# Optimization experiments

Measured on AMD Instinct MI355X. Metric: run time of the kernel, lower is better.

Reference implementation:

```python
import jax, jax.numpy as jnp
import numpy as np

B, T, C, H = 2, 2048, 1024, 16
HD = C // H            # 64
LAYER_IDX, N_LAYER = 5, 12
BASE = 16
# window_mode='power_2.0': progress=(5+1)/12=0.5; window=max(16, int(16+0.5**2*(2048-16)))=524
WINDOW = max(BASE, int(BASE + ((LAYER_IDX + 1) / N_LAYER) ** 2.0 * (T - BASE)))
WINDOW = min(WINDOW, T)


def setup_inputs() -> dict:
    key = jax.random.key(0)
    ks = jax.random.split(key, 6)
    x = jax.random.normal(ks[0], (B, T, C), dtype=jnp.float32)
    Wq = jax.random.normal(ks[1], (C, C), dtype=jnp.float32) * 0.02
    Wk = jax.random.normal(ks[2], (C, C), dtype=jnp.float32) * 0.02
    Wv = jax.random.normal(ks[3], (C, C), dtype=jnp.float32) * 0.02
    Wo = jax.random.normal(ks[4], (C, C), dtype=jnp.float32) * 0.02
    # RoPE tables: angles theta_i = t / 10000^(i/(HD/2)), shape (T,1,HD//2) to broadcast over (B,T,H,HD//2)
    half = HD // 2
    inv_freq = 1.0 / (10000.0 ** (jnp.arange(half, dtype=jnp.float32) / half))
    ang = jnp.arange(T, dtype=jnp.float32)[:, None] * inv_freq[None, :]  # (T, half)
    rope_cos = jnp.cos(ang)[:, None, :]  # (T,1,half)
    rope_sin = jnp.sin(ang)[:, None, :]
    return {"x": x, "Wq": Wq, "Wk": Wk, "Wv": Wv, "Wo": Wo,
            "rope_cos": rope_cos, "rope_sin": rope_sin}


def _apply_rotary(x, cos, sin):
    d = x.shape[-1] // 2
    x1, x2 = x[..., :d], x[..., d:]
    return jnp.concatenate([x1 * cos + x2 * sin, -x2 * sin + x1 * cos], axis=-1)


def reference(x, Wq, Wk, Wv, Wo, rope_cos, rope_sin):
    Bv, Tv, Cv = x.shape
    q = (x @ Wq).reshape(Bv, Tv, H, HD)
    k = (x @ Wk).reshape(Bv, Tv, H, HD)
    v = (x @ Wv).reshape(Bv, Tv, H, HD)
    q = _apply_rotary(q, rope_cos, rope_sin)
    k = _apply_rotary(k, rope_cos, rope_sin)
    # sliding-window causal mask: cols<=rows and cols>=rows-WINDOW+1
    rows = jnp.arange(Tv)[:, None]
    cols = jnp.arange(Tv)[None, :]
    allowed = (cols <= rows) & (cols >= rows - WINDOW + 1)  # (T,T)
    scale = 1.0 / np.sqrt(HD)
    scores = jnp.einsum('bthd,bshd->bhts', q, k) * scale  # (B,H,T,T)
    scores = jnp.where(allowed[None, None], scores, -jnp.inf)
    attn = jax.nn.softmax(scores, axis=-1)
    y = jnp.einsum('bhts,bshd->bthd', attn, v).reshape(Bv, Tv, Cv)
    return y @ Wo
```

## Files before the change

kernel.cpp:

```cpp
#include <hip/hip_runtime.h>
#include <math.h>

typedef unsigned short u16;
typedef unsigned int u32;
typedef __bf16 bf16x8 __attribute__((ext_vector_type(8)));
typedef float f32x4 __attribute__((ext_vector_type(4)));
typedef unsigned short ushort4v __attribute__((ext_vector_type(4)));

#define T_SEQ 2048
#define WIN_M1 523
#define QSCALE 0.180336879f
#define MASKV -1e30f

__device__ __forceinline__ u16 f2b(float f) {
  union { float f; unsigned int u; } v; v.f = f;
  unsigned int u = v.u;
  u += 0x7FFFu + ((u >> 16) & 1u);
  return (u16)(u >> 16);
}

__device__ __forceinline__ u32 cvtpk(float lo, float hi) {
  u32 r;
  asm("v_cvt_pk_bf16_f32 %0, %1, %2" : "=v"(r) : "v"(lo), "v"(hi));
  return r;
}

__device__ __forceinline__ void load_lds16(const u16* g, u16* l) {
  __builtin_amdgcn_global_load_lds(
      (const __attribute__((address_space(1))) void*)g,
      (__attribute__((address_space(3))) void*)l, 16, 0, 0);
}

__global__ void prep_k(const float* __restrict__ x, u16* __restrict__ xb,
                       const float* __restrict__ W0, const float* __restrict__ W1,
                       const float* __restrict__ W2, const float* __restrict__ W3,
                       u16* __restrict__ WcatT, u16* __restrict__ WoT) {
  const int bid = blockIdx.x;
  if (bid < 4096) {
    int i = bid * 256 + threadIdx.x;
    float4 v = ((const float4*)x)[i];
    u16* d = xb + i * 4;
    d[0] = f2b(v.x); d[1] = f2b(v.y); d[2] = f2b(v.z); d[3] = f2b(v.w);
    return;
  }
  __shared__ float tile[32][33];
  const int t = bid - 4096;
  const int z = t >> 10, i = t & 1023;
  const float* W = (z == 0) ? W0 : (z == 1) ? W1 : (z == 2) ? W2 : W3;
  u16* Wt = (z < 3) ? (WcatT + (size_t)z * 1024 * 1024) : WoT;
  int tx = threadIdx.x & 31, ty = threadIdx.x >> 5;
  int n0 = (i & 31) * 32, k0 = (i >> 5) * 32;
#pragma unroll
  for (int j = 0; j < 4; ++j)
    tile[ty + j * 8][tx] = W[(size_t)(k0 + ty + j * 8) * 1024 + n0 + tx];
  __syncthreads();
#pragma unroll
  for (int j = 0; j < 4; ++j)
    Wt[(size_t)(n0 + ty + j * 8) * 1024 + k0 + tx] = f2b(tile[tx][ty + j * 8]);
}

template <int MODE>
__global__ __launch_bounds__(256, 4) void gemm_k(
    const u16* __restrict__ A, const u16* __restrict__ Bt,
    float* __restrict__ outf,
    u16* __restrict__ Qo, u16* __restrict__ Ko, u16* __restrict__ Vto,
    const float* __restrict__ rc, const float* __restrict__ rs) {
  __shared__ alignas(16) u16 As[2][128 * 32];
  __shared__ alignas(16) u16 Bs[2][128 * 32];
  const int tid = threadIdx.x, lane = tid & 63, w = tid >> 6;
  const int l15 = lane & 15, q4 = lane >> 4;
  const int row0 = blockIdx.y * 128, col0 = blockIdx.x * 128;
  const int wm = w >> 1, wn = w & 1;
  constexpr int NT = 32;

  f32x4 acc[4][4];
#pragma unroll
  for (int i = 0; i < 4; ++i)
#pragma unroll
    for (int j = 0; j < 4; ++j) acc[i][j] = (f32x4){0.f, 0.f, 0.f, 0.f};

  const int off0 = (w * 2) * 1024 + lane * 16;
  const int r0 = off0 >> 6, c0 = (off0 & 63) >> 1;
  const int off1 = off0 + 1024;
  const int r1 = off1 >> 6, c1 = (off1 & 63) >> 1;
  const u16* gA0 = A + (size_t)(row0 + r0) * 1024 + c0;
  const u16* gA1 = A + (size_t)(row0 + r1) * 1024 + c1;
  const u16* gB0 = Bt + (size_t)(col0 + r0) * 1024 + c0;
  const u16* gB1 = Bt + (size_t)(col0 + r1) * 1024 + c1;
  const int soff = (w * 2) * 512;

  auto stage = [&](int buf, int t) {
    const int k0 = t * 32;
    load_lds16(gA0 + k0, &As[buf][soff]);
    load_lds16(gA1 + k0, &As[buf][soff + 512]);
    load_lds16(gB0 + k0, &Bs[buf][soff]);
    load_lds16(gB1 + k0, &Bs[buf][soff + 512]);
  };
  auto compute = [&](int buf) {
    bf16x8 af[4], bfr[4];
#pragma unroll
    for (int im = 0; im < 4; ++im)
      af[im] = *(const bf16x8*)&As[buf][(wm * 64 + im * 16 + l15) * 32 + q4 * 8];
#pragma unroll
    for (int jn = 0; jn < 4; ++jn)
      bfr[jn] = *(const bf16x8*)&Bs[buf][(wn * 64 + jn * 16 + l15) * 32 + q4 * 8];
#pragma unroll
    for (int im = 0; im < 4; ++im)
#pragma unroll
      for (int jn = 0; jn < 4; ++jn)
        acc[im][jn] = __builtin_amdgcn_mfma_f32_16x16x32_bf16(af[im], bfr[jn], acc[im][jn], 0, 0, 0);
  };

  stage(0, 0);
  for (int t = 0; t + 1 < NT; ++t) {
    stage((t + 1) & 1, t + 1);
    asm volatile("s_waitcnt vmcnt(4)" ::: "memory");
    __builtin_amdgcn_s_barrier();
    compute(t & 1);
    __builtin_amdgcn_s_barrier();
  }
  asm volatile("s_waitcnt vmcnt(0)" ::: "memory");
  __builtin_amdgcn_s_barrier();
  compute((NT - 1) & 1);

  if constexpr (MODE == 0) {
#pragma unroll
    for (int im = 0; im < 4; ++im) {
      const int rowb = row0 + wm * 64 + im * 16 + q4 * 4;
      const int b = rowb >> 11, t0 = rowb & 2047;
#pragma unroll
      for (int jn = 0; jn < 2; ++jn) {
        const int n = col0 + wn * 64 + jn * 16 + l15;
        const int sel = n >> 10, nn = n & 1023;
        const int h = nn >> 6, hd = nn & 63;
        if (sel < 2) {
          const float qs = (sel == 0) ? QSCALE : 1.0f;
          u16* dst = (sel == 0 ? Qo : Ko) + ((size_t)(b * 16 + h) * 2048) * 64;
#pragma unroll
          for (int r = 0; r < 4; ++r) {
            const int tt = t0 + r;
            const float c = rc[tt * 32 + hd], s = rs[tt * 32 + hd];
            const float x1 = acc[im][jn][r], x2 = acc[im][jn + 2][r];
            dst[(size_t)tt * 64 + hd] = f2b((x1 * c + x2 * s) * qs);
            dst[(size_t)tt * 64 + hd + 32] = f2b((x1 * c - x2 * s) * qs);
          }
        } else {
          ushort4v p1, p2;
#pragma unroll
          for (int r = 0; r < 4; ++r) {
            p1[r] = f2b(acc[im][jn][r]);
            p2[r] = f2b(acc[im][jn + 2][r]);
          }
          u16* dst = Vto + (size_t)(b * 16 + h) * 64 * 2048 + t0;
          *(ushort4v*)(dst + (size_t)hd * 2048) = p1;
          *(ushort4v*)(dst + (size_t)(hd + 32) * 2048) = p2;
        }
      }
    }
  } else {
#pragma unroll
    for (int im = 0; im < 4; ++im) {
      const int rowb = row0 + wm * 64 + im * 16 + q4 * 4;
#pragma unroll
      for (int jn = 0; jn < 4; ++jn) {
        const int n = col0 + wn * 64 + jn * 16 + l15;
#pragma unroll
        for (int r = 0; r < 4; ++r)
          outf[(size_t)(rowb + r) * 1024 + n] = acc[im][jn][r];
      }
    }
  }
}

__global__ __launch_bounds__(256) void attn_k(
    const u16* __restrict__ Q, const u16* __restrict__ Kk,
    const u16* __restrict__ Vt, u16* __restrict__ Y) {
  const int lane = threadIdx.x & 63, w = threadIdx.x >> 6;
  const int l15 = lane & 15, q4 = lane >> 4;
  const int hw = blockIdx.x;
  const int work = (hw & 7) * 64 + (hw >> 3);
  const int bh = work >> 4;
  const int qt = 15 - (work & 15);
  const int q0 = qt * 128 + w * 32;
  const u16* Qb = Q + (size_t)bh * 2048 * 64;
  const u16* Kb = Kk + (size_t)bh * 2048 * 64;
  const u16* Vb = Vt + (size_t)bh * 64 * 2048;

  bf16x8 bq[2][2];
#pragma unroll
  for (int qs = 0; qs < 2; ++qs)
#pragma unroll
    for (int kb = 0; kb < 2; ++kb)
      bq[qs][kb] = *(const bf16x8*)(Qb + (size_t)(q0 + qs * 16 + l15) * 64 + kb * 32 + q4 * 8);

  f32x4 o[2][4];
#pragma unroll
  for (int qs = 0; qs < 2; ++qs)
#pragma unroll
    for (int jo = 0; jo < 4; ++jo) o[qs][jo] = (f32x4){0.f, 0.f, 0.f, 0.f};
  float lp[2] = {0.f, 0.f};

  int s0 = q0 - WIN_M1; if (s0 < 0) s0 = 0; s0 &= ~31;
  const int srcA = l15 + ((q4 & 1) << 5);
  const int srcB = srcA + 16;
  const bool lowq4 = (q4 < 2);

  bf16x8 kc[2][2], kn[2][2];
  bf16x8 vc[4], vn[4];
#pragma unroll
  for (int ks = 0; ks < 2; ++ks)
#pragma unroll
    for (int kb = 0; kb < 2; ++kb)
      kc[ks][kb] = *(const bf16x8*)(Kb + (size_t)(s0 + ks * 16 + l15) * 64 + kb * 32 + q4 * 8);
#pragma unroll
  for (int jo = 0; jo < 4; ++jo)
    vc[jo] = *(const bf16x8*)(Vb + (size_t)(jo * 16 + l15) * 2048 + s0 + q4 * 8);

  int kv0 = s0;

#define TILE_BODY(KC, VC, KN, VN)                                                      \
  {                                                                                    \
    const int kvn = kv0 + 32;                                                          \
    if (kvn <= q0) {                                                                   \
      _Pragma("unroll") for (int ks = 0; ks < 2; ++ks)                                 \
          _Pragma("unroll") for (int kb = 0; kb < 2; ++kb)                             \
              KN[ks][kb] = *(const bf16x8*)(Kb + (size_t)(kvn + ks * 16 + l15) * 64 +  \
                                            kb * 32 + q4 * 8);                         \
      _Pragma("unroll") for (int jo = 0; jo < 4; ++jo)                                 \
          VN[jo] = *(const bf16x8*)(Vb + (size_t)(jo * 16 + l15) * 2048 + kvn +        \
                                    q4 * 8);                                           \
    }                                                                                  \
    f32x4 ss[2][2];                                                                    \
    _Pragma("unroll") for (int ks = 0; ks < 2; ++ks)                                   \
        _Pragma("unroll") for (int qs = 0; qs < 2; ++qs)                               \
            ss[ks][qs] = (f32x4){0.f, 0.f, 0.f, 0.f};                                  \
    _Pragma("unroll") for (int kb = 0; kb < 2; ++kb)                                   \
        _Pragma("unroll") for (int ks = 0; ks < 2; ++ks)                               \
            _Pragma("unroll") for (int qs = 0; qs < 2; ++qs)                           \
                ss[ks][qs] = __builtin_amdgcn_mfma_f32_16x16x32_bf16(                  \
                    KC[ks][kb], bq[qs][kb], ss[ks][qs], 0, 0, 0);                      \
    if ((kv0 + 32 > q0) || (kv0 < q0 - 492)) {                                         \
      _Pragma("unroll") for (int qs = 0; qs < 2; ++qs) {                               \
        const int tq = q0 + qs * 16 + l15;                                             \
        _Pragma("unroll") for (int ks = 0; ks < 2; ++ks)                               \
            _Pragma("unroll") for (int r = 0; r < 4; ++r) {                            \
          const int kv = kv0 + ks * 16 + q4 * 4 + r;                                   \
          if (kv > tq || kv < tq - WIN_M1) ss[ks][qs][r] = MASKV;                      \
        }                                                                              \
      }                                                                                \
    }                                                                                  \
    _Pragma("unroll") for (int qs = 0; qs < 2; ++qs) {                                 \
      float p[2][4];                                                                   \
      _Pragma("unroll") for (int ks = 0; ks < 2; ++ks)                                 \
          _Pragma("unroll") for (int r = 0; r < 4; ++r)                                \
              p[ks][r] = exp2f(ss[ks][qs][r]);                                         \
      lp[qs] += ((p[0][0] + p[0][1]) + (p[0][2] + p[0][3])) +                          \
                ((p[1][0] + p[1][1]) + (p[1][2] + p[1][3]));                           \
      const u32 a0 = cvtpk(p[0][0], p[0][1]), a1 = cvtpk(p[0][2], p[0][3]);            \
      const u32 b0 = cvtpk(p[1][0], p[1][1]), b1 = cvtpk(p[1][2], p[1][3]);            \
      union { u32 d[4]; bf16x8 v; } pu;                                                \
      const u32 d0a = (u32)__shfl((int)a0, srcA), d0b = (u32)__shfl((int)b0, srcA);    \
      const u32 d1a = (u32)__shfl((int)a1, srcA), d1b = (u32)__shfl((int)b1, srcA);    \
      const u32 d2a = (u32)__shfl((int)a0, srcB), d2b = (u32)__shfl((int)b0, srcB);    \
      const u32 d3a = (u32)__shfl((int)a1, srcB), d3b = (u32)__shfl((int)b1, srcB);    \
      pu.d[0] = lowq4 ? d0a : d0b;                                                     \
      pu.d[1] = lowq4 ? d1a : d1b;                                                     \
      pu.d[2] = lowq4 ? d2a : d2b;                                                     \
      pu.d[3] = lowq4 ? d3a : d3b;                                                     \
      _Pragma("unroll") for (int jo = 0; jo < 4; ++jo)                                 \
          o[qs][jo] = __builtin_amdgcn_mfma_f32_16x16x32_bf16(pu.v, VC[jo],            \
                                                              o[qs][jo], 0, 0, 0);     \
    }                                                                                  \
  }

  while (true) {
    TILE_BODY(kc, vc, kn, vn);
    kv0 += 32; if (kv0 > q0) break;
    TILE_BODY(kn, vn, kc, vc);
    kv0 += 32; if (kv0 > q0) break;
  }
#undef TILE_BODY

  const int b = bh >> 4, h = bh & 15;
  u16* Yb = Y + (size_t)(b * 2048 + q0) * 1024 + h * 64 + l15;
#pragma unroll
  for (int qs = 0; qs < 2; ++qs) {
    float l = lp[qs];
    l += __shfl_xor(l, 16);
    l += __shfl_xor(l, 32);
#pragma unroll
    for (int r = 0; r < 4; ++r) {
      const float lv = __shfl(l, q4 * 4 + r);
      const float inv = 1.0f / lv;
      u16* yr = Yb + (size_t)(qs * 16 + q4 * 4 + r) * 1024;
#pragma unroll
      for (int jo = 0; jo < 4; ++jo) yr[jo * 16] = f2b(o[qs][jo][r] * inv);
    }
  }
}

extern "C" void kernel_launch(void* const* d_in, const int* in_sizes, int n_in,
                              void* d_out, int out_size, void* d_ws, size_t ws_size,
                              hipStream_t stream) {
  const float* x = (const float*)d_in[0];
  const float* Wq = (const float*)d_in[1];
  const float* Wk = (const float*)d_in[2];
  const float* Wv = (const float*)d_in[3];
  const float* Wo = (const float*)d_in[4];
  const float* rc = (const float*)d_in[5];
  const float* rs = (const float*)d_in[6];
  float* out = (float*)d_out;
  char* ws = (char*)d_ws;
  const size_t MB = 1024 * 1024;
  u16* xb = (u16*)(ws);
  u16* WcatT = (u16*)(ws + 8 * MB);
  u16* WoT = (u16*)(ws + 14 * MB);
  u16* Qr = (u16*)(ws + 16 * MB);
  u16* Kr = (u16*)(ws + 24 * MB);
  u16* Vt = (u16*)(ws + 32 * MB);
  u16* Y = (u16*)(ws + 40 * MB);

  prep_k<<<8192, 256, 0, stream>>>(x, xb, Wq, Wk, Wv, Wo, WcatT, WoT);
  gemm_k<0><<<dim3(24, 32), 256, 0, stream>>>(xb, WcatT, nullptr, Qr, Kr, Vt, rc, rs);
  attn_k<<<512, 256, 0, stream>>>(Qr, Kr, Vt, Y);
  gemm_k<1><<<dim3(8, 32), 256, 0, stream>>>(Y, WoT, out, nullptr, nullptr, nullptr, nullptr, nullptr);
}
```

Baseline: 108.3 us.

## Split attention KV range across two blocks and triple-buffer GEMM LDS

Attention work is split into two halves of the key range per query tile, doubling the grid; each half writes unnormalized bf16 partial outputs and row sums, and a new combine kernel adds them and normalizes. This targets low occupancy and load imbalance in the attention kernel. The GEMM mainloop moves from double to triple LDS buffering with deeper prefetch to hide global load latency. The cost is an extra kernel launch, extra memory traffic, bf16 rounding of partial sums, and more LDS per GEMM block.

```diff
diff --git a/kernel.cpp b/kernel.cpp
--- a/kernel.cpp
+++ b/kernel.cpp
@@ -6,6 +6,7 @@
 typedef __bf16 bf16x8 __attribute__((ext_vector_type(8)));
 typedef float f32x4 __attribute__((ext_vector_type(4)));
 typedef unsigned short ushort4v __attribute__((ext_vector_type(4)));
+typedef unsigned short ushort8v __attribute__((ext_vector_type(8)));
 
 #define T_SEQ 2048
 #define WIN_M1 523
@@ -17,6 +18,12 @@
   unsigned int u = v.u;
   u += 0x7FFFu + ((u >> 16) & 1u);
   return (u16)(u >> 16);
+}
+
+__device__ __forceinline__ float b2f(u16 b) {
+  union { unsigned int u; float f; } v;
+  v.u = ((u32)b) << 16;
+  return v.f;
 }
 
 __device__ __forceinline__ u32 cvtpk(float lo, float hi) {
@@ -65,8 +72,8 @@
     float* __restrict__ outf,
     u16* __restrict__ Qo, u16* __restrict__ Ko, u16* __restrict__ Vto,
     const float* __restrict__ rc, const float* __restrict__ rs) {
-  __shared__ alignas(16) u16 As[2][128 * 32];
-  __shared__ alignas(16) u16 Bs[2][128 * 32];
+  __shared__ alignas(16) u16 As[3][128 * 32];
+  __shared__ alignas(16) u16 Bs[3][128 * 32];
   const int tid = threadIdx.x, lane = tid & 63, w = tid >> 6;
   const int l15 = lane & 15, q4 = lane >> 4;
   const int row0 = blockIdx.y * 128, col0 = blockIdx.x * 128;
@@ -112,16 +119,25 @@
   };
 
   stage(0, 0);
-  for (int t = 0; t + 1 < NT; ++t) {
-    stage((t + 1) & 1, t + 1);
-    asm volatile("s_waitcnt vmcnt(4)" ::: "memory");
+  stage(1, 1);
+  int bs = 2, bc = 0;
+  for (int t = 0; t + 2 < NT; ++t) {
+    stage(bs, t + 2);
+    asm volatile("s_waitcnt vmcnt(8)" ::: "memory");
     __builtin_amdgcn_s_barrier();
-    compute(t & 1);
+    compute(bc);
     __builtin_amdgcn_s_barrier();
-  }
+    bs = (bs + 1 == 3) ? 0 : bs + 1;
+    bc = (bc + 1 == 3) ? 0 : bc + 1;
+  }
+  asm volatile("s_waitcnt vmcnt(4)" ::: "memory");
+  __builtin_amdgcn_s_barrier();
+  compute(bc);
+  __builtin_amdgcn_s_barrier();
+  bc = (bc + 1 == 3) ? 0 : bc + 1;
   asm volatile("s_waitcnt vmcnt(0)" ::: "memory");
   __builtin_amdgcn_s_barrier();
-  compute((NT - 1) & 1);
+  compute(bc);
 
   if constexpr (MODE == 0) {
 #pragma unroll
@@ -174,13 +190,17 @@
 
 __global__ __launch_bounds__(256) void attn_k(
     const u16* __restrict__ Q, const u16* __restrict__ Kk,
-    const u16* __restrict__ Vt, u16* __restrict__ Y) {
+    const u16* __restrict__ Vt, u16* __restrict__ Yraw, u16* __restrict__ oP1,
+    float* __restrict__ lP) {
   const int lane = threadIdx.x & 63, w = threadIdx.x >> 6;
   const int l15 = lane & 15, q4 = lane >> 4;
   const int hw = blockIdx.x;
-  const int work = (hw & 7) * 64 + (hw >> 3);
-  const int bh = work >> 4;
-  const int qt = 15 - (work & 15);
+  const int w128 = hw >> 3;
+  const int half = w128 & 1;
+  const int wk = w128 >> 1;
+  const int bhl = wk >> 4;
+  const int bh = (hw & 7) * 4 + bhl;
+  const int qt = (wk + 3 * bhl) & 15;
   const int q0 = qt * 128 + w * 32;
   const u16* Qb = Q + (size_t)bh * 2048 * 64;
   const u16* Kb = Kk + (size_t)bh * 2048 * 64;
@@ -201,27 +221,32 @@
   float lp[2] = {0.f, 0.f};
 
   int s0 = q0 - WIN_M1; if (s0 < 0) s0 = 0; s0 &= ~31;
+  const int n = ((q0 - s0) >> 5) + 1;
+  const int nA = (n + 1) >> 1;
+  const int kvStart = (half == 0) ? s0 : s0 + nA * 32;
+  const int kvEnd = (half == 0) ? s0 + (nA - 1) * 32 : q0;
   const int srcA = l15 + ((q4 & 1) << 5);
   const int srcB = srcA + 16;
   const bool lowq4 = (q4 < 2);
 
   bf16x8 kc[2][2], kn[2][2];
   bf16x8 vc[4], vn[4];
-#pragma unroll
-  for (int ks = 0; ks < 2; ++ks)
-#pragma unroll
-    for (int kb = 0; kb < 2; ++kb)
-      kc[ks][kb] = *(const bf16x8*)(Kb + (size_t)(s0 + ks * 16 + l15) * 64 + kb * 32 + q4 * 8);
-#pragma unroll
-  for (int jo = 0; jo < 4; ++jo)
-    vc[jo] = *(const bf16x8*)(Vb + (size_t)(jo * 16 + l15) * 2048 + s0 + q4 * 8);
-
-  int kv0 = s0;
+  int kv0 = kvStart;
+
+  if (kv0 <= kvEnd) {
+#pragma unroll
+    for (int ks = 0; ks < 2; ++ks)
+#pragma unroll
+      for (int kb = 0; kb < 2; ++kb)
+        kc[ks][kb] = *(const bf16x8*)(Kb + (size_t)(kv0 + ks * 16 + l15) * 64 + kb * 32 + q4 * 8);
+#pragma unroll
+    for (int jo = 0; jo < 4; ++jo)
+      vc[jo] = *(const bf16x8*)(Vb + (size_t)(jo * 16 + l15) * 2048 + kv0 + q4 * 8);
 
 #define TILE_BODY(KC, VC, KN, VN)                                                      \
   {                                                                                    \
     const int kvn = kv0 + 32;                                                          \
-    if (kvn <= q0) {                                                                   \
+    if (kvn <= kvEnd) {                                                                \
       _Pragma("unroll") for (int ks = 0; ks < 2; ++ks)                                 \
           _Pragma("unroll") for (int kb = 0; kb < 2; ++kb)                             \
               KN[ks][kb] = *(const bf16x8*)(Kb + (size_t)(kvn + ks * 16 + l15) * 64 +  \
@@ -273,30 +298,48 @@
     }                                                                                  \
   }
 
-  while (true) {
-    TILE_BODY(kc, vc, kn, vn);
-    kv0 += 32; if (kv0 > q0) break;
-    TILE_BODY(kn, vn, kc, vc);
-    kv0 += 32; if (kv0 > q0) break;
-  }
+    while (true) {
+      TILE_BODY(kc, vc, kn, vn);
+      kv0 += 32; if (kv0 > kvEnd) break;
+      TILE_BODY(kn, vn, kc, vc);
+      kv0 += 32; if (kv0 > kvEnd) break;
+    }
 #undef TILE_BODY
+  }
 
   const int b = bh >> 4, h = bh & 15;
-  u16* Yb = Y + (size_t)(b * 2048 + q0) * 1024 + h * 64 + l15;
+  u16* dstO = (half == 0) ? Yraw : oP1;
+  u16* Yb = dstO + (size_t)(b * 2048 + q0) * 1024 + h * 64 + l15;
+  float* lD = lP + (size_t)half * 65536 + bh * 2048 + q0;
 #pragma unroll
   for (int qs = 0; qs < 2; ++qs) {
     float l = lp[qs];
     l += __shfl_xor(l, 16);
     l += __shfl_xor(l, 32);
+    if (q4 == 0) lD[qs * 16 + l15] = l;
 #pragma unroll
     for (int r = 0; r < 4; ++r) {
-      const float lv = __shfl(l, q4 * 4 + r);
-      const float inv = 1.0f / lv;
       u16* yr = Yb + (size_t)(qs * 16 + q4 * 4 + r) * 1024;
 #pragma unroll
-      for (int jo = 0; jo < 4; ++jo) yr[jo * 16] = f2b(o[qs][jo][r] * inv);
+      for (int jo = 0; jo < 4; ++jo) yr[jo * 16] = f2b(o[qs][jo][r]);
     }
   }
+}
+
+__global__ void combine_k(u16* __restrict__ Y, const u16* __restrict__ oP1,
+                          const float* __restrict__ lP) {
+  const int i8 = (blockIdx.x * 256 + threadIdx.x) * 8;
+  const int row = i8 >> 10, col = i8 & 1023;
+  const int b = row >> 11, t = row & 2047, h = col >> 6;
+  const int bh = b * 16 + h;
+  const float l0 = lP[bh * 2048 + t], l1 = lP[65536 + bh * 2048 + t];
+  const float inv = 1.0f / (l0 + l1);
+  ushort8v a = *(const ushort8v*)(Y + i8);
+  ushort8v c = *(const ushort8v*)(oP1 + i8);
+  ushort8v y;
+#pragma unroll
+  for (int j = 0; j < 8; ++j) y[j] = f2b((b2f(a[j]) + b2f(c[j])) * inv);
+  *(ushort8v*)(Y + i8) = y;
 }
 
 extern "C" void kernel_launch(void* const* d_in, const int* in_sizes, int n_in,
@@ -319,9 +362,12 @@
   u16* Kr = (u16*)(ws + 24 * MB);
   u16* Vt = (u16*)(ws + 32 * MB);
   u16* Y = (u16*)(ws + 40 * MB);
+  u16* oP1 = xb;
+  float* lP = (float*)(ws + 8 * MB);
 
   prep_k<<<8192, 256, 0, stream>>>(x, xb, Wq, Wk, Wv, Wo, WcatT, WoT);
   gemm_k<0><<<dim3(24, 32), 256, 0, stream>>>(xb, WcatT, nullptr, Qr, Kr, Vt, rc, rs);
-  attn_k<<<512, 256, 0, stream>>>(Qr, Kr, Vt, Y);
+  attn_k<<<1024, 256, 0, stream>>>(Qr, Kr, Vt, Y, oP1, lP);
+  combine_k<<<2048, 256, 0, stream>>>(Y, oP1, lP);
   gemm_k<1><<<dim3(8, 32), 256, 0, stream>>>(Y, WoT, out, nullptr, nullptr, nullptr, nullptr, nullptr);
 }
```

After: 116.7 us. 1.08x slower.
